# Kernel tuning notes

Hardware: AMD Instinct MI355X
Metric: run time of the kernel (lower is better)

## Reference

```python
import jax, jax.numpy as jnp
import numpy as np

B, S, H, NH, L, V, P = 2, 1024, 768, 12, 4, 32000, 1024
HD = H // NH  # head dim = 64; matches scale_val = hidden/num_heads


def setup_inputs() -> dict:
    key = jax.random.key(0)
    ks = jax.random.split(key, 18)
    sc = 0.02
    n = jax.random.normal
    return {
        "input_ids": jax.random.randint(ks[0], (B, S), 0, V, dtype=jnp.int32),
        "seq_mask": jnp.ones((B, S), jnp.float32),
        "bpe_emb": (n(ks[1], (V, H)) * sc).astype(jnp.float32),
        "pos_emb": (n(ks[2], (P, H)) * sc).astype(jnp.float32),
        "qkv_w": (n(ks[3], (L, H, 3 * H)) * sc).astype(jnp.float32),
        "qkv_b": jnp.zeros((L, 3 * H), jnp.float32),
        "res_w": (n(ks[4], (L, H, H)) * sc).astype(jnp.float32),
        "res_b": jnp.zeros((L, H), jnp.float32),
        "ln1_g": jnp.ones((L, H), jnp.float32),
        "ln1_b": jnp.zeros((L, H), jnp.float32),
        "ff1_w": (n(ks[5], (L, H, 4 * H)) * sc).astype(jnp.float32),
        "ff1_b": jnp.zeros((L, 4 * H), jnp.float32),
        "ff2_w": (n(ks[6], (L, 4 * H, H)) * sc).astype(jnp.float32),
        "ff2_b": jnp.zeros((L, H), jnp.float32),
        "ln2_g": jnp.ones((L, H), jnp.float32),
        "ln2_b": jnp.zeros((L, H), jnp.float32),
        "pred_w": (n(ks[7], (H, V)) * sc).astype(jnp.float32),
    }


def _layer_norm(x, g, b, e=1e-5):
    u = jnp.mean(x, -1, keepdims=True)
    s = jnp.mean((x - u) ** 2, -1, keepdims=True)
    return g * ((x - u) / jnp.sqrt(s + e)) + b


def _attention(x, seq_mask, w_qkv, b_qkv, w_res, b_res):
    qkv = x @ w_qkv + b_qkv                    # [B,S,3H]
    q, k, v = jnp.split(qkv, 3, axis=-1)
    q = q.reshape(B, S, NH, HD)
    k = k.reshape(B, S, NH, HD)
    v = v.reshape(B, S, NH, HD)
    score = jnp.einsum('bqhd,bkhd->bhqk', q, k) / jnp.sqrt(jnp.float32(HD))
    tril = jnp.tril(jnp.ones((S, S), jnp.float32))           # causal
    mask = tril[None, None] * seq_mask[:, None, None, :]      # [B,1,S,S]
    score = score + (1.0 - mask) * -1e9
    prob = jax.nn.softmax(score, axis=-1)      # dropout rate 0 -> identity
    val = jnp.einsum('bhqk,bkhd->bqhd', prob, v).reshape(B, S, H)
    return val @ w_res + b_res                 # dropout rate 0 -> identity


def reference(input_ids, seq_mask, bpe_emb, pos_emb, qkv_w, qkv_b, res_w, res_b,
              ln1_g, ln1_b, ff1_w, ff1_b, ff2_w, ff2_b, ln2_g, ln2_b, pred_w):
    pos_idx = jnp.arange(S)
    h = bpe_emb[input_ids] + pos_emb[pos_idx][None]           # [B,S,H]
    for l in range(L):
        a = _attention(h, seq_mask, qkv_w[l], qkv_b[l], res_w[l], res_b[l])
        h = _layer_norm(h + a, ln1_g[l], ln1_b[l])
        m = (jax.nn.gelu(h @ ff1_w[l] + ff1_b[l], approximate=False)
             @ ff2_w[l] + ff2_b[l])
        h = _layer_norm(h + m, ln2_g[l], ln2_b[l])
    pred_score = h @ pred_w                                   # [B,S,V]
    pred_prob = jax.nn.softmax(pred_score, axis=-1)
    return pred_score, pred_prob
```

## Files before the change

### kernel.cpp

```cpp
#include <hip/hip_runtime.h>
#include <math.h>

#define BB 2
#define SS 1024
#define HH 768
#define NHEAD 12
#define HDIM 64
#define NLAYER 4
#define VV 32000
#define MROWS (BB*SS)

typedef unsigned short u16;
typedef __attribute__((ext_vector_type(8))) short short8;
typedef __attribute__((ext_vector_type(4))) float f32x4;
typedef __attribute__((ext_vector_type(4))) unsigned short u16x4;

__device__ __forceinline__ u16 f2bf(float f) {
    union { float f; unsigned u; } x; x.f = f;
    unsigned r = (x.u + 0x7fff + ((x.u >> 16) & 1)) >> 16;
    return (u16)r;
}
__device__ __forceinline__ float bf2f(u16 b) {
    union { unsigned u; float f; } x; x.u = ((unsigned)b) << 16;
    return x.f;
}

__device__ __forceinline__ void gload_lds16(const u16* g, u16* l) {
    __builtin_amdgcn_global_load_lds((const __attribute__((address_space(1))) void*)g,
                                     (__attribute__((address_space(3))) void*)l, 16, 0, 0);
}

__global__ __launch_bounds__(256) void conv_transpose(
    const float* __restrict__ W, u16* __restrict__ Wt, int K, int N) {
    int l = blockIdx.z;
    W  += (size_t)l * K * N;
    Wt += (size_t)l * K * N;
    __shared__ u16 tile[32][33];
    int k0 = blockIdx.y * 32, n0 = blockIdx.x * 32;
    int t = threadIdx.x;
    int ky = t >> 3, nx = (t & 7) * 4;
    float4 v = *(const float4*)(W + (size_t)(k0 + ky) * N + n0 + nx);
    tile[nx + 0][ky] = f2bf(v.x);
    tile[nx + 1][ky] = f2bf(v.y);
    tile[nx + 2][ky] = f2bf(v.z);
    tile[nx + 3][ky] = f2bf(v.w);
    __syncthreads();
    int nr = t >> 3, kc = (t & 7) * 4;
    u16x4 o;
    o[0] = tile[nr][kc + 0]; o[1] = tile[nr][kc + 1];
    o[2] = tile[nr][kc + 2]; o[3] = tile[nr][kc + 3];
    *(u16x4*)(Wt + (size_t)(n0 + nr) * K + k0 + kc) = o;
}

__global__ void embed_kernel(const int* __restrict__ ids,
                             const float* __restrict__ bpe,
                             const float* __restrict__ pos,
                             float* __restrict__ h, u16* __restrict__ hb) {
    int row = blockIdx.x;
    int s = row % SS;
    int id = ids[row];
    const float4* br = (const float4*)(bpe + (size_t)id * HH);
    const float4* pr = (const float4*)(pos + (size_t)s * HH);
    float4* hr = (float4*)(h + (size_t)row * HH);
    u16x4* hbr = (u16x4*)(hb + (size_t)row * HH);
    int t = threadIdx.x;
    float4 a = br[t], c = pr[t];
    a.x += c.x; a.y += c.y; a.z += c.z; a.w += c.w;
    hr[t] = a;
    u16x4 u; u[0] = f2bf(a.x); u[1] = f2bf(a.y); u[2] = f2bf(a.z); u[3] = f2bf(a.w);
    hbr[t] = u;
}

template<int BM, int ACT, int WF32, int WBF>
__global__ __launch_bounds__(256) void mfma_gemm(
    const u16* __restrict__ A, const u16* __restrict__ Wt,
    const float* __restrict__ bias, float* __restrict__ C,
    u16* __restrict__ Cb, int M, int N, int K) {
    constexpr int MR = BM / 32;
    __shared__ u16 As[BM * 32];
    __shared__ u16 Bs[128 * 32];
    const int tid = threadIdx.x;
    const int lane = tid & 63;
    const int wid = tid >> 6;

    const int nwg = gridDim.x * gridDim.y;
    int id = blockIdx.x + gridDim.x * blockIdx.y;
    int id2 = (nwg & 7) ? id : ((id & 7) * (nwg >> 3) + (id >> 3));
    const int brow = (id2 % gridDim.x) * BM;
    const int bcol = (id2 / gridDim.x) * 128;

    const int wr = (wid >> 1) * (BM / 2);
    const int wc = (wid & 1) * 64;
    f32x4 acc[MR][4] = {};

    const u16* Abase = A + (size_t)brow * K;
    const u16* Bbase = Wt + (size_t)bcol * K;
    const int lrow = lane & 15;
    const int lk = (lane >> 4) * 8;

    for (int kt = 0; kt < K; kt += 32) {
        __syncthreads();
#pragma unroll
        for (int c0 = 0; c0 < BM * 4; c0 += 256) {
            int c = c0 + tid;
            int r = c >> 2, off = (c & 3) * 8;
            gload_lds16(Abase + (size_t)r * K + kt + off, As + c * 8);
        }
#pragma unroll
        for (int c0 = 0; c0 < 512; c0 += 256) {
            int c = c0 + tid;
            int r = c >> 2, off = (c & 3) * 8;
            gload_lds16(Bbase + (size_t)r * K + kt + off, Bs + c * 8);
        }
        __syncthreads();
        short8 a[MR], b[4];
#pragma unroll
        for (int m = 0; m < MR; ++m)
            a[m] = *(const short8*)(As + (wr + m * 16 + lrow) * 32 + lk);
#pragma unroll
        for (int n = 0; n < 4; ++n)
            b[n] = *(const short8*)(Bs + (wc + n * 16 + lrow) * 32 + lk);
#pragma unroll
        for (int m = 0; m < MR; ++m)
#pragma unroll
            for (int n = 0; n < 4; ++n)
                acc[m][n] = __builtin_amdgcn_mfma_f32_16x16x32_bf16(a[m], b[n], acc[m][n], 0, 0, 0);
    }

    const int lr4 = (lane >> 4) * 4;
#pragma unroll
    for (int n = 0; n < 4; ++n) {
        int col = bcol + wc + n * 16 + lrow;
        float bv = bias ? bias[col] : 0.f;
#pragma unroll
        for (int m = 0; m < MR; ++m) {
#pragma unroll
            for (int j = 0; j < 4; ++j) {
                int row = brow + wr + m * 16 + lr4 + j;
                float v = acc[m][n][j] + bv;
                if (ACT == 1) v = 0.5f * v * (1.f + erff(v * 0.70710678118654752f));
                if (WF32) C[(size_t)row * N + col] = v;
                if (WBF)  Cb[(size_t)row * N + col] = f2bf(v);
            }
        }
    }
}

__global__ __launch_bounds__(256) void attn_kernel(
    const u16* __restrict__ qkvb, const float* __restrict__ seq_mask,
    u16* __restrict__ av) {
    __shared__ u16 Ks[64 * 64];
    __shared__ u16 Vt[64 * 64];
    __shared__ u16 Ps[64 * 64];
    const int qb = blockIdx.x, hd = blockIdx.y, b = blockIdx.z;
    const int t = threadIdx.x;
    const int lane = t & 63;
    const int w = t >> 6;
    const int lrow = lane & 15;
    const int lhi = lane >> 4;
    const int q0 = qb * 64;
    const size_t rs = 3 * HH;

    short8 aq[2];
    {
        const u16* qrow = qkvb + (size_t)(b * SS + q0 + w * 16 + lrow) * rs + hd * HDIM;
        aq[0] = *(const short8*)(qrow + lhi * 8);
        aq[1] = *(const short8*)(qrow + 32 + lhi * 8);
    }

    f32x4 o[4] = {};
    float m_[4] = {-INFINITY, -INFINITY, -INFINITY, -INFINITY};
    float l_[4] = {0.f, 0.f, 0.f, 0.f};

    for (int kt = 0; kt <= qb; ++kt) {
        const int k0 = kt * 64;
        __syncthreads();
        {
            const int kr = t >> 2, dc = t & 3;
            const u16* kbase = qkvb + (size_t)(b * SS + k0 + kr) * rs + HH + hd * HDIM + dc * 16;
            short8 kA = *(const short8*)(kbase);
            short8 kB = *(const short8*)(kbase + 8);
            char* krowp = (char*)Ks + kr * 128;
            *(short8*)(krowp + (((dc * 32 + 0)  ^ ((kr & 7) << 4)))) = kA;
            *(short8*)(krowp + (((dc * 32 + 16) ^ ((kr & 7) << 4)))) = kB;

            const u16* vbase = kbase + HH;
            short8 vA = *(const short8*)(vbase);
            short8 vB = *(const short8*)(vbase + 8);
#pragma unroll
            for (int e = 0; e < 8; ++e) {
                int d0 = dc * 16 + e;
                int d1 = dc * 16 + 8 + e;
                *(u16*)((char*)Vt + d0 * 128 + ((kr * 2) ^ ((d0 & 7) << 4))) = (u16)vA[e];
                *(u16*)((char*)Vt + d1 * 128 + ((kr * 2) ^ ((d1 & 7) << 4))) = (u16)vB[e];
            }
        }
        __syncthreads();

        f32x4 s[4] = {};
        __builtin_amdgcn_s_setprio(1);
#pragma unroll
        for (int n = 0; n < 4; ++n) {
            const int krow = n * 16 + lrow;
            char* kp = (char*)Ks + krow * 128;
#pragma unroll
            for (int c = 0; c < 2; ++c) {
                short8 bk = *(const short8*)(kp + ((c * 64 + lhi * 16) ^ ((krow & 7) << 4)));
                s[n] = __builtin_amdgcn_mfma_f32_16x16x32_bf16(aq[c], bk, s[n], 0, 0, 0);
            }
        }
        __builtin_amdgcn_s_setprio(0);

        float sm[4];
#pragma unroll
        for (int n = 0; n < 4; ++n) sm[n] = seq_mask[b * SS + k0 + n * 16 + lrow];
        const int diag = (kt == qb);
#pragma unroll
        for (int j = 0; j < 4; ++j) {
            const int qglob = q0 + w * 16 + lhi * 4 + j;
            float sv[4];
#pragma unroll
            for (int n = 0; n < 4; ++n) {
                const int kglob = k0 + n * 16 + lrow;
                float msk = (diag && kglob > qglob) ? 0.f : sm[n];
                sv[n] = s[n][j] * 0.125f + (1.f - msk) * (-1e9f);
            }
            float tm = fmaxf(fmaxf(sv[0], sv[1]), fmaxf(sv[2], sv[3]));
            tm = fmaxf(tm, __shfl_xor(tm, 1));
            tm = fmaxf(tm, __shfl_xor(tm, 2));
            tm = fmaxf(tm, __shfl_xor(tm, 4));
            tm = fmaxf(tm, __shfl_xor(tm, 8));
            float mn = fmaxf(m_[j], tm);
            float sc = __expf(m_[j] - mn);
            float ps = 0.f;
#pragma unroll
            for (int n = 0; n < 4; ++n) {
                float p = __expf(sv[n] - mn);
                s[n][j] = p;
                ps += p;
            }
            ps += __shfl_xor(ps, 1);
            ps += __shfl_xor(ps, 2);
            ps += __shfl_xor(ps, 4);
            ps += __shfl_xor(ps, 8);
            l_[j] = l_[j] * sc + ps;
            m_[j] = mn;
#pragma unroll
            for (int dn = 0; dn < 4; ++dn) o[dn][j] *= sc;
        }

#pragma unroll
        for (int j = 0; j < 4; ++j) {
            const int prow = w * 16 + lhi * 4 + j;
            char* pp = (char*)Ps + prow * 128;
#pragma unroll
            for (int n = 0; n < 4; ++n)
                *(u16*)(pp + ((n * 32 + lrow * 2) ^ ((prow & 7) << 4))) = f2bf(s[n][j]);
        }

        const int arow = w * 16 + lrow;
        char* ap_p = (char*)Ps + arow * 128;
        __builtin_amdgcn_s_setprio(1);
#pragma unroll
        for (int c = 0; c < 2; ++c) {
            short8 ap = *(const short8*)(ap_p + ((c * 64 + lhi * 16) ^ ((arow & 7) << 4)));
#pragma unroll
            for (int dn = 0; dn < 4; ++dn) {
                const int vrow = dn * 16 + lrow;
                short8 bv = *(const short8*)((char*)Vt + vrow * 128 +
                                             ((c * 64 + lhi * 16) ^ ((vrow & 7) << 4)));
                o[dn] = __builtin_amdgcn_mfma_f32_16x16x32_bf16(ap, bv, o[dn], 0, 0, 0);
            }
        }
        __builtin_amdgcn_s_setprio(0);
    }

#pragma unroll
    for (int j = 0; j < 4; ++j) {
        const int q = q0 + w * 16 + lhi * 4 + j;
        const float inv = 1.f / l_[j];
        u16* orow = av + (size_t)(b * SS + q) * HH + hd * HDIM;
#pragma unroll
        for (int dn = 0; dn < 4; ++dn)
            orow[dn * 16 + lrow] = f2bf(o[dn][j] * inv);
    }
}

__global__ void add_ln_kernel(float* __restrict__ h, u16* __restrict__ hb,
                              const float* __restrict__ a,
                              const float* __restrict__ g,
                              const float* __restrict__ bta) {
    int row = blockIdx.x;
    int t = threadIdx.x;
    __shared__ float red[256];
    size_t base = (size_t)row * HH;
    float x0 = h[base + t]       + a[base + t];
    float x1 = h[base + t + 256] + a[base + t + 256];
    float x2 = h[base + t + 512] + a[base + t + 512];

    red[t] = x0 + x1 + x2;
    __syncthreads();
    for (int o = 128; o; o >>= 1) { if (t < o) red[t] += red[t + o]; __syncthreads(); }
    float mean = red[0] * (1.0f / 768.0f);
    __syncthreads();

    float d0 = x0 - mean, d1 = x1 - mean, d2 = x2 - mean;
    red[t] = d0 * d0 + d1 * d1 + d2 * d2;
    __syncthreads();
    for (int o = 128; o; o >>= 1) { if (t < o) red[t] += red[t + o]; __syncthreads(); }
    float var = red[0] * (1.0f / 768.0f);
    float inv = 1.0f / sqrtf(var + 1e-5f);

    float y0 = g[t]       * d0 * inv + bta[t];
    float y1 = g[t + 256] * d1 * inv + bta[t + 256];
    float y2 = g[t + 512] * d2 * inv + bta[t + 512];
    h[base + t] = y0;       hb[base + t] = f2bf(y0);
    h[base + t + 256] = y1; hb[base + t + 256] = f2bf(y1);
    h[base + t + 512] = y2; hb[base + t + 512] = f2bf(y2);
}

__global__ __launch_bounds__(256) void softmax_v_kernel(
    const float* __restrict__ score, float* __restrict__ prob) {
    __shared__ u16 srow[VV];
    __shared__ float red[256];
    int row = blockIdx.x;
    int t = threadIdx.x;
    const float4* sr = (const float4*)(score + (size_t)row * VV);
    float4* pr = (float4*)(prob + (size_t)row * VV);
    const int n4 = VV / 4;

    float mx = -INFINITY;
    for (int i = t; i < n4; i += 256) {
        float4 v = sr[i];
        u16x4 u; u[0] = f2bf(v.x); u[1] = f2bf(v.y); u[2] = f2bf(v.z); u[3] = f2bf(v.w);
        *(u16x4*)(srow + i * 4) = u;
        mx = fmaxf(mx, fmaxf(fmaxf(bf2f(u[0]), bf2f(u[1])), fmaxf(bf2f(u[2]), bf2f(u[3]))));
    }
    red[t] = mx; __syncthreads();
    for (int o = 128; o; o >>= 1) { if (t < o) red[t] = fmaxf(red[t], red[t + o]); __syncthreads(); }
    mx = red[0];
    __syncthreads();

    float s = 0.f;
    for (int i = t; i < n4; i += 256) {
        u16x4 u = *(const u16x4*)(srow + i * 4);
        s += __expf(bf2f(u[0]) - mx) + __expf(bf2f(u[1]) - mx)
           + __expf(bf2f(u[2]) - mx) + __expf(bf2f(u[3]) - mx);
    }
    red[t] = s; __syncthreads();
    for (int o = 128; o; o >>= 1) { if (t < o) red[t] += red[t + o]; __syncthreads(); }
    float inv = 1.0f / red[0];

    for (int i = t; i < n4; i += 256) {
        u16x4 u = *(const u16x4*)(srow + i * 4);
        float4 o4;
        o4.x = __expf(bf2f(u[0]) - mx) * inv; o4.y = __expf(bf2f(u[1]) - mx) * inv;
        o4.z = __expf(bf2f(u[2]) - mx) * inv; o4.w = __expf(bf2f(u[3]) - mx) * inv;
        pr[i] = o4;
    }
}

extern "C" void kernel_launch(void* const* d_in, const int* in_sizes, int n_in,
                              void* d_out, int out_size, void* d_ws, size_t ws_size,
                              hipStream_t stream) {
    const int*   ids      = (const int*)d_in[0];
    const float* seq_mask = (const float*)d_in[1];
    const float* bpe      = (const float*)d_in[2];
    const float* pos      = (const float*)d_in[3];
    const float* qkv_w    = (const float*)d_in[4];
    const float* qkv_b    = (const float*)d_in[5];
    const float* res_w    = (const float*)d_in[6];
    const float* res_b    = (const float*)d_in[7];
    const float* ln1_g    = (const float*)d_in[8];
    const float* ln1_b    = (const float*)d_in[9];
    const float* ff1_w    = (const float*)d_in[10];
    const float* ff1_b    = (const float*)d_in[11];
    const float* ff2_w    = (const float*)d_in[12];
    const float* ff2_b    = (const float*)d_in[13];
    const float* ln2_g    = (const float*)d_in[14];
    const float* ln2_b    = (const float*)d_in[15];
    const float* pred_w   = (const float*)d_in[16];

    float* out_score = (float*)d_out;
    float* out_prob  = out_score + (size_t)MROWS * VV;

    size_t off = 0;
    auto take = [&](size_t bytes) -> size_t {
        size_t p = off; off += (bytes + 255) & ~(size_t)255; return p;
    };
    const size_t o_qkvT = take((size_t)NLAYER * HH * 3 * HH * 2);
    const size_t o_resT = take((size_t)NLAYER * HH * HH * 2);
    const size_t o_ff1T = take((size_t)NLAYER * HH * 4 * HH * 2);
    const size_t o_ff2T = take((size_t)NLAYER * 4 * HH * HH * 2);
    const size_t o_predT = take((size_t)HH * VV * 2);
    const size_t o_h    = take((size_t)MROWS * HH * 4);
    const size_t o_a    = take((size_t)MROWS * HH * 4);
    const size_t o_qkvb = take((size_t)MROWS * 3 * HH * 2);
    const size_t o_hb   = take((size_t)MROWS * HH * 2);
    const size_t o_avb  = take((size_t)MROWS * HH * 2);
    const size_t o_midb = take((size_t)MROWS * 4 * HH * 2);
    const size_t need = off;

    char* arena = (ws_size >= need) ? (char*)d_ws : (char*)out_prob;
    u16*   qkvT = (u16*)(arena + o_qkvT);
    u16*   resT = (u16*)(arena + o_resT);
    u16*   ff1T = (u16*)(arena + o_ff1T);
    u16*   ff2T = (u16*)(arena + o_ff2T);
    u16*   predT = (u16*)(arena + o_predT);
    float* h    = (float*)(arena + o_h);
    float* a    = (float*)(arena + o_a);
    u16*   qkvb = (u16*)(arena + o_qkvb);
    u16*   hb   = (u16*)(arena + o_hb);
    u16*   avb  = (u16*)(arena + o_avb);
    u16*   midb = (u16*)(arena + o_midb);

    conv_transpose<<<dim3(3 * HH / 32, HH / 32, NLAYER), 256, 0, stream>>>(qkv_w, qkvT, HH, 3 * HH);
    conv_transpose<<<dim3(HH / 32, HH / 32, NLAYER), 256, 0, stream>>>(res_w, resT, HH, HH);
    conv_transpose<<<dim3(4 * HH / 32, HH / 32, NLAYER), 256, 0, stream>>>(ff1_w, ff1T, HH, 4 * HH);
    conv_transpose<<<dim3(HH / 32, 4 * HH / 32, NLAYER), 256, 0, stream>>>(ff2_w, ff2T, 4 * HH, HH);
    conv_transpose<<<dim3(VV / 32, HH / 32, 1), 256, 0, stream>>>(pred_w, predT, HH, VV);

    embed_kernel<<<MROWS, 192, 0, stream>>>(ids, bpe, pos, h, hb);

    for (int l = 0; l < NLAYER; ++l) {
        mfma_gemm<128, 0, 0, 1><<<dim3(MROWS / 128, 3 * HH / 128), 256, 0, stream>>>(
            hb, qkvT + (size_t)l * HH * 3 * HH, qkv_b + (size_t)l * 3 * HH,
            nullptr, qkvb, MROWS, 3 * HH, HH);
        attn_kernel<<<dim3(SS / 64, NHEAD, BB), 256, 0, stream>>>(qkvb, seq_mask, avb);
        mfma_gemm<64, 0, 1, 0><<<dim3(MROWS / 64, HH / 128), 256, 0, stream>>>(
            avb, resT + (size_t)l * HH * HH, res_b + (size_t)l * HH,
            a, nullptr, MROWS, HH, HH);
        add_ln_kernel<<<MROWS, 256, 0, stream>>>(h, hb, a,
            ln1_g + (size_t)l * HH, ln1_b + (size_t)l * HH);
        mfma_gemm<128, 1, 0, 1><<<dim3(MROWS / 128, 4 * HH / 128), 256, 0, stream>>>(
            hb, ff1T + (size_t)l * HH * 4 * HH, ff1_b + (size_t)l * 4 * HH,
            nullptr, midb, MROWS, 4 * HH, HH);
        mfma_gemm<64, 0, 1, 0><<<dim3(MROWS / 64, HH / 128), 256, 0, stream>>>(
            midb, ff2T + (size_t)l * 4 * HH * HH, ff2_b + (size_t)l * HH,
            a, nullptr, MROWS, HH, 4 * HH);
        add_ln_kernel<<<MROWS, 256, 0, stream>>>(h, hb, a,
            ln2_g + (size_t)l * HH, ln2_b + (size_t)l * HH);
    }

    mfma_gemm<128, 0, 1, 0><<<dim3(MROWS / 128, VV / 128), 256, 0, stream>>>(
        hb, predT, nullptr, out_score, nullptr, MROWS, VV, HH);
    softmax_v_kernel<<<MROWS, 256, 0, stream>>>(out_score, out_prob);
}
```

Baseline: 1.140 ms.

## Double-buffer GEMM LDS tiles, prefetch attention K/V, widen vocab softmax blocks

The GEMM now double-buffers its A/B shared-memory tiles, issuing the next k-tile's global-to-LDS loads before computing the current one and waiting with explicit vmcnt counts. The attention kernel reverses the query-block order so the longest causal blocks start first, and prefetches the next K/V tile into registers while the current tile is being computed. The vocab softmax moves from 256 to 512 threads per row. The changes are meant to hide global load latency and reduce tail imbalance. In exchange they double GEMM LDS use, which can lower occupancy, and they rely on hand-written vmcnt values being correct.

```diff
diff --git a/kernel.cpp b/kernel.cpp
--- a/kernel.cpp
+++ b/kernel.cpp
@@ -77,8 +77,8 @@
     const float* __restrict__ bias, float* __restrict__ C,
     u16* __restrict__ Cb, int M, int N, int K) {
     constexpr int MR = BM / 32;
-    __shared__ u16 As[BM * 32];
-    __shared__ u16 Bs[128 * 32];
+    __shared__ u16 As[2 * BM * 32];
+    __shared__ u16 Bs[2 * 128 * 32];
     const int tid = threadIdx.x;
     const int lane = tid & 63;
     const int wid = tid >> 6;
@@ -98,33 +98,52 @@
     const int lrow = lane & 15;
     const int lk = (lane >> 4) * 8;
 
-    for (int kt = 0; kt < K; kt += 32) {
-        __syncthreads();
+    auto stage = [&](u16* Ad, u16* Bd, int kt) {
 #pragma unroll
         for (int c0 = 0; c0 < BM * 4; c0 += 256) {
             int c = c0 + tid;
             int r = c >> 2, off = (c & 3) * 8;
-            gload_lds16(Abase + (size_t)r * K + kt + off, As + c * 8);
+            gload_lds16(Abase + (size_t)r * K + kt + off, Ad + c * 8);
         }
 #pragma unroll
         for (int c0 = 0; c0 < 512; c0 += 256) {
             int c = c0 + tid;
             int r = c >> 2, off = (c & 3) * 8;
-            gload_lds16(Bbase + (size_t)r * K + kt + off, Bs + c * 8);
-        }
-        __syncthreads();
+            gload_lds16(Bbase + (size_t)r * K + kt + off, Bd + c * 8);
+        }
+    };
+
+    const int nt = K / 32;
+    stage(As, Bs, 0);
+    for (int t = 0; t < nt; ++t) {
+        u16* Ac = As + (t & 1) * (BM * 32);
+        u16* Bc = Bs + (t & 1) * (128 * 32);
+        if (t + 1 < nt) {
+            stage(As + ((t + 1) & 1) * (BM * 32),
+                  Bs + ((t + 1) & 1) * (128 * 32), (t + 1) * 32);
+            if constexpr (BM == 128) asm volatile("s_waitcnt vmcnt(4)" ::: "memory");
+            else                     asm volatile("s_waitcnt vmcnt(3)" ::: "memory");
+        } else {
+            asm volatile("s_waitcnt vmcnt(0)" ::: "memory");
+        }
+        __builtin_amdgcn_s_barrier();
+        __builtin_amdgcn_sched_barrier(0);
+
         short8 a[MR], b[4];
 #pragma unroll
         for (int m = 0; m < MR; ++m)
-            a[m] = *(const short8*)(As + (wr + m * 16 + lrow) * 32 + lk);
+            a[m] = *(const short8*)(Ac + (wr + m * 16 + lrow) * 32 + lk);
 #pragma unroll
         for (int n = 0; n < 4; ++n)
-            b[n] = *(const short8*)(Bs + (wc + n * 16 + lrow) * 32 + lk);
+            b[n] = *(const short8*)(Bc + (wc + n * 16 + lrow) * 32 + lk);
 #pragma unroll
         for (int m = 0; m < MR; ++m)
 #pragma unroll
             for (int n = 0; n < 4; ++n)
                 acc[m][n] = __builtin_amdgcn_mfma_f32_16x16x32_bf16(a[m], b[n], acc[m][n], 0, 0, 0);
+
+        __builtin_amdgcn_sched_barrier(0);
+        __builtin_amdgcn_s_barrier();
     }
 
     const int lr4 = (lane >> 4) * 4;
@@ -152,7 +171,8 @@
     __shared__ u16 Ks[64 * 64];
     __shared__ u16 Vt[64 * 64];
     __shared__ u16 Ps[64 * 64];
-    const int qb = blockIdx.x, hd = blockIdx.y, b = blockIdx.z;
+    const int qb = gridDim.x - 1 - blockIdx.x;
+    const int hd = blockIdx.y, b = blockIdx.z;
     const int t = threadIdx.x;
     const int lane = t & 63;
     const int w = t >> 6;
@@ -172,21 +192,23 @@
     float m_[4] = {-INFINITY, -INFINITY, -INFINITY, -INFINITY};
     float l_[4] = {0.f, 0.f, 0.f, 0.f};
 
+    const int kr = t >> 2, dc = t & 3;
+    short8 kA, kB, vA, vB;
+    {
+        const u16* kbase = qkvb + (size_t)(b * SS + kr) * rs + HH + hd * HDIM + dc * 16;
+        kA = *(const short8*)(kbase);
+        kB = *(const short8*)(kbase + 8);
+        vA = *(const short8*)(kbase + HH);
+        vB = *(const short8*)(kbase + HH + 8);
+    }
+
     for (int kt = 0; kt <= qb; ++kt) {
         const int k0 = kt * 64;
         __syncthreads();
         {
-            const int kr = t >> 2, dc = t & 3;
-            const u16* kbase = qkvb + (size_t)(b * SS + k0 + kr) * rs + HH + hd * HDIM + dc * 16;
-            short8 kA = *(const short8*)(kbase);
-            short8 kB = *(const short8*)(kbase + 8);
             char* krowp = (char*)Ks + kr * 128;
             *(short8*)(krowp + (((dc * 32 + 0)  ^ ((kr & 7) << 4)))) = kA;
             *(short8*)(krowp + (((dc * 32 + 16) ^ ((kr & 7) << 4)))) = kB;
-
-            const u16* vbase = kbase + HH;
-            short8 vA = *(const short8*)(vbase);
-            short8 vB = *(const short8*)(vbase + 8);
 #pragma unroll
             for (int e = 0; e < 8; ++e) {
                 int d0 = dc * 16 + e;
@@ -196,6 +218,14 @@
             }
         }
         __syncthreads();
+
+        if (kt < qb) {
+            const u16* kbase = qkvb + (size_t)(b * SS + k0 + 64 + kr) * rs + HH + hd * HDIM + dc * 16;
+            kA = *(const short8*)(kbase);
+            kB = *(const short8*)(kbase + 8);
+            vA = *(const short8*)(kbase + HH);
+            vB = *(const short8*)(kbase + HH + 8);
+        }
 
         f32x4 s[4] = {};
         __builtin_amdgcn_s_setprio(1);
@@ -319,10 +349,10 @@
     h[base + t + 512] = y2; hb[base + t + 512] = f2bf(y2);
 }
 
-__global__ __launch_bounds__(256) void softmax_v_kernel(
+__global__ __launch_bounds__(512) void softmax_v_kernel(
     const float* __restrict__ score, float* __restrict__ prob) {
     __shared__ u16 srow[VV];
-    __shared__ float red[256];
+    __shared__ float red[512];
     int row = blockIdx.x;
     int t = threadIdx.x;
     const float4* sr = (const float4*)(score + (size_t)row * VV);
@@ -330,28 +360,28 @@
     const int n4 = VV / 4;
 
     float mx = -INFINITY;
-    for (int i = t; i < n4; i += 256) {
+    for (int i = t; i < n4; i += 512) {
         float4 v = sr[i];
         u16x4 u; u[0] = f2bf(v.x); u[1] = f2bf(v.y); u[2] = f2bf(v.z); u[3] = f2bf(v.w);
         *(u16x4*)(srow + i * 4) = u;
         mx = fmaxf(mx, fmaxf(fmaxf(bf2f(u[0]), bf2f(u[1])), fmaxf(bf2f(u[2]), bf2f(u[3]))));
     }
     red[t] = mx; __syncthreads();
-    for (int o = 128; o; o >>= 1) { if (t < o) red[t] = fmaxf(red[t], red[t + o]); __syncthreads(); }
+    for (int o = 256; o; o >>= 1) { if (t < o) red[t] = fmaxf(red[t], red[t + o]); __syncthreads(); }
     mx = red[0];
     __syncthreads();
 
     float s = 0.f;
-    for (int i = t; i < n4; i += 256) {
+    for (int i = t; i < n4; i += 512) {
         u16x4 u = *(const u16x4*)(srow + i * 4);
         s += __expf(bf2f(u[0]) - mx) + __expf(bf2f(u[1]) - mx)
            + __expf(bf2f(u[2]) - mx) + __expf(bf2f(u[3]) - mx);
     }
     red[t] = s; __syncthreads();
-    for (int o = 128; o; o >>= 1) { if (t < o) red[t] += red[t + o]; __syncthreads(); }
+    for (int o = 256; o; o >>= 1) { if (t < o) red[t] += red[t + o]; __syncthreads(); }
     float inv = 1.0f / red[0];
 
-    for (int i = t; i < n4; i += 256) {
+    for (int i = t; i < n4; i += 512) {
         u16x4 u = *(const u16x4*)(srow + i * 4);
         float4 o4;
         o4.x = __expf(bf2f(u[0]) - mx) * inv; o4.y = __expf(bf2f(u[1]) - mx) * inv;
@@ -444,5 +474,5 @@
 
     mfma_gemm<128, 0, 1, 0><<<dim3(MROWS / 128, VV / 128), 256, 0, stream>>>(
         hb, predT, nullptr, out_score, nullptr, MROWS, VV, HH);
-    softmax_v_kernel<<<MROWS, 256, 0, stream>>>(out_score, out_prob);
-}
+    softmax_v_kernel<<<MROWS, 512, 0, stream>>>(out_score, out_prob);
+}
```

Result: faster. 1.106 ms (-3.0%).
